# Optimization experiments

Measured on AMD Instinct MI355X. Metric: run time of the kernel, lower is better.

Reference implementation:

```python
import jax, jax.numpy as jnp
import numpy as np


def _three_nn(xyz1, xyz2):
    # xyz1: [B,N1,3], xyz2: [B,N2,3]
    # Squared euclidean distances, as in the original three_nn CUDA/TF op.
    d2 = (jnp.sum(xyz1 * xyz1, axis=-1)[:, :, None]
          + jnp.sum(xyz2 * xyz2, axis=-1)[:, None, :]
          - 2.0 * jnp.einsum('bnd,bmd->bnm', xyz1, xyz2))  # [B,N1,N2]
    neg_vals, idx = jax.lax.top_k(-d2, 3)                 # 3 smallest
    return -neg_vals, idx                                  # dist [B,N1,3], idx [B,N1,3]


def reference(xyz1, xyz2, points1, points2, w1, w2):
    dist, idx = _three_nn(xyz1, xyz2)
    dist = jnp.maximum(dist, 1e-10)
    inv = 1.0 / dist                                       # [B,N1,3]
    weight = inv / jnp.sum(inv, axis=2, keepdims=True)     # [B,N1,3]

    B = points2.shape[0]
    b_idx = jnp.arange(B)[:, None, None]
    gathered = points2[b_idx, idx]                         # [B,N1,3,C2]
    interpolated = jnp.einsum('bnk,bnkc->bnc', weight, gathered)  # [B,N1,C2]

    new_points = jnp.concatenate([interpolated, points1], axis=2)  # [B,N1,C2+C1]

    # 1x1 conv MLP = per-point matmul; bn=False, activation=relu on all layers
    h = jax.nn.relu(jnp.einsum('bnc,cf->bnf', new_points, w1))
    h = jax.nn.relu(jnp.einsum('bnc,cf->bnf', h, w2))
    return h


def setup_inputs() -> dict:
    key = jax.random.key(0)
    k1, k2, k3, k4, k5, k6 = jax.random.split(key, 6)
    B, N1, N2, C1, C2 = 4, 8192, 2048, 128, 256
    xyz1 = jax.random.normal(k1, (B, N1, 3), dtype=jnp.float32)
    xyz2 = jax.random.normal(k2, (B, N2, 3), dtype=jnp.float32)
    points1 = jax.random.normal(k3, (B, N1, C1), dtype=jnp.float32)
    points2 = jax.random.normal(k4, (B, N2, C2), dtype=jnp.float32)
    # glorot-normal-ish init for the 1x1 conv kernels
    w1 = jax.random.normal(k5, (C2 + C1, 256), dtype=jnp.float32) * (2.0 / (C2 + C1 + 256)) ** 0.5
    w2 = jax.random.normal(k6, (256, 256), dtype=jnp.float32) * (2.0 / (256 + 256)) ** 0.5
    return {"xyz1": xyz1, "xyz2": xyz2, "points1": points1, "points2": points2, "w1": w1, "w2": w2}
```

## Files before the change

### kernel.cpp

```cpp
#include <hip/hip_runtime.h>
#include <stdint.h>

typedef unsigned short u16;
typedef unsigned int   u32;

#define NB 4
#define N1 8192
#define N2 2048
#define C1 128
#define C2 256
#define KK1 384
#define FF 256
#define TM 64
#define NTHR 1024
#define NCH 16
#define CHSZ (N2 / NCH)
#define TILES_PER_B (N1 / TM)
#define APAD 400
#define HPAD 272
#define NKT1 (KK1 / 32)
#define NKT2 (FF / 32)
#define ABYTES (TM * APAD * 2)
#define PDOFF  ABYTES
#define PIOFF  (ABYTES + NCH * TM * 3 * 4)

typedef short short8 __attribute__((ext_vector_type(8)));
typedef float floatx4 __attribute__((ext_vector_type(4)));
typedef float f32x2  __attribute__((ext_vector_type(2)));
typedef u32   u32x4  __attribute__((ext_vector_type(4)));

union ABFrag { u32 u[4]; short8 v; u32x4 q; };

__device__ __forceinline__ u16 f2b(float f) {
    u32 x = __float_as_uint(f);
    return (u16)((x + 0x7FFFu + ((x >> 16) & 1u)) >> 16);
}
__device__ __forceinline__ u32 pack2(float a, float b) {
    return (u32)f2b(a) | ((u32)f2b(b) << 16);
}

__global__ __launch_bounds__(256) void prep_kernel(
    const float* __restrict__ w1, const float* __restrict__ w2,
    const float* __restrict__ xyz2,
    u32x4* __restrict__ w1F, u32x4* __restrict__ w2F, float* __restrict__ xq)
{
    int i = blockIdx.x * 256 + threadIdx.x;
    if (i < 16 * NKT1 * 64) {
        int nt = i / (NKT1 * 64), rem = i % (NKT1 * 64);
        int kt = rem / 64, lane = rem % 64;
        int n  = nt * 16 + (lane & 15);
        int k0 = kt * 32 + (lane >> 4) * 8;
        const float* wc = w1 + n;
        ABFrag f;
        f.u[0] = pack2(wc[(k0 + 0) * FF], wc[(k0 + 1) * FF]);
        f.u[1] = pack2(wc[(k0 + 2) * FF], wc[(k0 + 3) * FF]);
        f.u[2] = pack2(wc[(k0 + 4) * FF], wc[(k0 + 5) * FF]);
        f.u[3] = pack2(wc[(k0 + 6) * FF], wc[(k0 + 7) * FF]);
        w1F[i] = f.q;
        return;
    }
    i -= 16 * NKT1 * 64;
    if (i < 16 * NKT2 * 64) {
        int nt = i / (NKT2 * 64), rem = i % (NKT2 * 64);
        int kt = rem / 64, lane = rem % 64;
        int n  = nt * 16 + (lane & 15);
        int k0 = kt * 32 + (lane >> 4) * 8;
        const float* wc = w2 + n;
        ABFrag f;
        f.u[0] = pack2(wc[(k0 + 0) * FF], wc[(k0 + 1) * FF]);
        f.u[1] = pack2(wc[(k0 + 2) * FF], wc[(k0 + 3) * FF]);
        f.u[2] = pack2(wc[(k0 + 4) * FF], wc[(k0 + 5) * FF]);
        f.u[3] = pack2(wc[(k0 + 6) * FF], wc[(k0 + 7) * FF]);
        w2F[i] = f.q;
        return;
    }
    i -= 16 * NKT2 * 64;
    if (i < NB * N2) {
        const float* q = xyz2 + (size_t)i * 3;
        float x = q[0], y = q[1], z = q[2];
        float s2 = __fadd_rn(__fadd_rn(__fmul_rn(x,x), __fmul_rn(y,y)), __fmul_rn(z,z));
        int p = i >> 1, e = i & 1;
        float* rec = xq + (size_t)p * 8;
        rec[0 + e] = -2.0f * x;
        rec[2 + e] = -2.0f * y;
        rec[4 + e] = -2.0f * z;
        rec[6 + e] = s2;
    }
}

__global__ __launch_bounds__(NTHR, 8) void fp_fused_kernel(
    const float* __restrict__ xyz1, const float* __restrict__ p1,
    const float* __restrict__ p2,
    const u32x4* __restrict__ w1F,  const u32x4* __restrict__ w2F,
    const float4* __restrict__ xq,  float* __restrict__ out)
{
    __shared__ int   s_idx[TM][3];
    __shared__ float s_wt[TM][3];
    __shared__ __align__(16) char s_buf[ABYTES + NCH * TM * 3 * 8];

    const int tid = threadIdx.x;
    const int b   = blockIdx.x / TILES_PER_B;
    const int t0  = (blockIdx.x % TILES_PER_B) * TM;

    u16*   A  = (u16*)s_buf;
    float* pd = (float*)(s_buf + PDOFF);
    int*   pi = (int*)(s_buf + PIOFF);

    {
        const int c4 = (tid & 31) * 4, r32 = tid >> 5;
        #pragma unroll
        for (int rv = 0; rv < 2; ++rv) {
            int rr = r32 + rv * 32;
            float4 v = *(const float4*)(p1 + ((size_t)b * N1 + t0 + rr) * C1 + c4);
            u32* w = (u32*)(A + rr * APAD + 256 + c4);
            w[0] = pack2(v.x, v.y);
            w[1] = pack2(v.z, v.w);
        }
    }

    {
        const int r  = tid & 63;
        const int ch = __builtin_amdgcn_readfirstlane(tid >> 6);
        const float4* cb = xq + ((size_t)b * (N2 / 2) + ch * (CHSZ / 2)) * 2;
        const float* q = xyz1 + ((size_t)b * N1 + t0 + r) * 3;
        float qx = q[0], qy = q[1], qz = q[2];
        float s1 = __fadd_rn(__fadd_rn(__fmul_rn(qx,qx), __fmul_rn(qy,qy)), __fmul_rn(qz,qz));
        float bd0 = 3e38f, bd1 = 3e38f, bd2 = 3e38f;
        int   bi0 = 0, bi1 = 0, bi2 = 0;
        const int j0 = ch * CHSZ;
        #pragma unroll 4
        for (int jj = 0; jj < CHSZ / 2; ++jj) {
            float4 f0 = cb[2 * jj];
            float4 f1 = cb[2 * jj + 1];
            f32x2 dpair;
            {
                #pragma clang fp contract(off)
                f32x2 qx2 = {qx, qx}, qy2 = {qy, qy}, qz2 = {qz, qz}, s1v = {s1, s1};
                f32x2 nx = {f0.x, f0.y}, ny = {f0.z, f0.w};
                f32x2 nz = {f1.x, f1.y}, ss = {f1.z, f1.w};
                f32x2 u  = qx2 * nx;
                f32x2 v  = qy2 * ny;
                f32x2 w  = u + v;
                f32x2 z2 = qz2 * nz;
                f32x2 t  = w + z2;
                f32x2 s12 = s1v + ss;
                dpair = s12 + t;
            }
            #pragma unroll
            for (int e = 0; e < 2; ++e) {
                float d = dpair[e];
                int   j = j0 + 2 * jj + e;
                float nb0 = fminf(d, bd0);
                float nb1 = __builtin_amdgcn_fmed3f(d, bd0, bd1);
                float nb2 = __builtin_amdgcn_fmed3f(d, bd1, bd2);
                bool c0 = d < bd0, c1 = d < bd1, c2 = d < bd2;
                int t01 = c0 ? bi0 : j;
                bi0     = c0 ? j   : bi0;
                int t12 = c1 ? bi1 : j;
                bi1     = c1 ? t01 : bi1;
                bi2     = c2 ? t12 : bi2;
                bd0 = nb0; bd1 = nb1; bd2 = nb2;
            }
        }
        const int o = (ch * TM + r) * 3;
        pd[o+0] = bd0; pd[o+1] = bd1; pd[o+2] = bd2;
        pi[o+0] = bi0; pi[o+1] = bi1; pi[o+2] = bi2;
    }
    __syncthreads();

    if (tid < TM) {
        float d0 = 3e38f, d1 = 3e38f, d2 = 3e38f;
        int   i0 = 0, i1 = 0, i2 = 0;
        for (int c = 0; c < NCH; ++c) {
            const int o = (c * TM + tid) * 3;
            #pragma unroll
            for (int k = 0; k < 3; ++k) {
                float d = pd[o + k]; int ix = pi[o + k];
                float n0 = fminf(d, d0);
                float n1 = __builtin_amdgcn_fmed3f(d, d0, d1);
                float n2 = __builtin_amdgcn_fmed3f(d, d1, d2);
                bool c0 = d < d0, c1 = d < d1, c2 = d < d2;
                int t01 = c0 ? i0 : ix;
                i0      = c0 ? ix : i0;
                int t12 = c1 ? i1 : t01;
                i1      = c1 ? t01 : i1;
                i2      = c2 ? t12 : i2;
                d0 = n0; d1 = n1; d2 = n2;
            }
        }
        d0 = fmaxf(d0, 1e-10f); d1 = fmaxf(d1, 1e-10f); d2 = fmaxf(d2, 1e-10f);
        float v0 = 1.0f / d0, v1 = 1.0f / d1, v2 = 1.0f / d2;
        float s  = 1.0f / (v0 + v1 + v2);
        s_wt[tid][0] = v0 * s; s_wt[tid][1] = v1 * s; s_wt[tid][2] = v2 * s;
        s_idx[tid][0] = i0; s_idx[tid][1] = i1; s_idx[tid][2] = i2;
    }
    __syncthreads();

    {
        const float* pb = p2 + (size_t)b * N2 * C2;
        const int col4 = (tid & 63) * 4;
        const int wvr  = tid >> 6;
        #pragma unroll
        for (int m = 0; m < 4; ++m) {
            int rr = wvr + m * 16;
            float w0 = s_wt[rr][0], w1v = s_wt[rr][1], w2v = s_wt[rr][2];
            int   i0 = s_idx[rr][0], i1 = s_idx[rr][1], i2 = s_idx[rr][2];
            float4 a0 = *(const float4*)(pb + (size_t)i0 * C2 + col4);
            float4 a1 = *(const float4*)(pb + (size_t)i1 * C2 + col4);
            float4 a2 = *(const float4*)(pb + (size_t)i2 * C2 + col4);
            float e0 = w0 * a0.x + w1v * a1.x + w2v * a2.x;
            float e1 = w0 * a0.y + w1v * a1.y + w2v * a2.y;
            float e2 = w0 * a0.z + w1v * a1.z + w2v * a2.z;
            float e3 = w0 * a0.w + w1v * a1.w + w2v * a2.w;
            u32* w = (u32*)(A + rr * APAD + col4);
            w[0] = pack2(e0, e1);
            w[1] = pack2(e2, e3);
        }
    }
    __syncthreads();

    const int lane = tid & 63;
    const int wv   = tid >> 6;
    const int lr   = lane & 15;
    const int lg   = lane >> 4;
    const int wvb  = wv * 16;

    int id1[4], id2[4];
    {
        u16 rbf = f2b((float)lr);
        u16 c32 = f2b(1.0f / 32.0f);
        ABFrag pa, pc;
        u32 ra = (u32)rbf | ((u32)rbf << 16);
        u32 rc = (u32)c32 | ((u32)c32 << 16);
        pa.u[0] = pa.u[1] = pa.u[2] = pa.u[3] = ra;
        pc.u[0] = pc.u[1] = pc.u[2] = pc.u[3] = rc;
        floatx4 z = {0.f, 0.f, 0.f, 0.f};
        floatx4 D1 = __builtin_amdgcn_mfma_f32_16x16x32_bf16(pa.v, pc.v, z, 0, 0, 0);
        floatx4 D2 = __builtin_amdgcn_mfma_f32_16x16x32_bf16(pc.v, pa.v, z, 0, 0, 0);
        #pragma unroll
        for (int g = 0; g < 4; ++g) { id1[g] = (int)(D1[g] + 0.5f); id2[g] = (int)(D2[g] + 0.5f); }
    }

    floatx4 acc[4];
    #pragma unroll
    for (int i = 0; i < 4; ++i) acc[i] = floatx4{0.f, 0.f, 0.f, 0.f};

    {
        const u32x4* wf = w1F + (size_t)(wv * NKT1) * 64 + lane;
        const int kb8 = lg * 8;
        for (int kk = 0; kk < NKT1; ++kk) {
            ABFrag bf; bf.q = wf[(size_t)kk * 64];
            ABFrag a[4];
            #pragma unroll
            for (int rt = 0; rt < 4; ++rt)
                a[rt].q = *(const u32x4*)(A + (rt * 16 + lr) * APAD + kk * 32 + kb8);
            #pragma unroll
            for (int rt = 0; rt < 4; ++rt)
                acc[rt] = __builtin_amdgcn_mfma_f32_16x16x32_bf16(a[rt].v, bf.v, acc[rt], 0, 0, 0);
        }
    }
    __syncthreads();

    u16* H = (u16*)s_buf;
    #pragma unroll
    for (int rt = 0; rt < 4; ++rt)
        #pragma unroll
        for (int g = 0; g < 4; ++g) {
            int row = rt * 16 + id1[g];
            int col = wvb + id2[g];
            H[row * HPAD + col] = f2b(fmaxf(acc[rt][g], 0.0f));
        }
    __syncthreads();

    floatx4 acc2[4];
    #pragma unroll
    for (int i = 0; i < 4; ++i) acc2[i] = floatx4{0.f, 0.f, 0.f, 0.f};

    {
        const u32x4* wf = w2F + (size_t)(wv * NKT2) * 64 + lane;
        const int kb8 = lg * 8;
        for (int kk = 0; kk < NKT2; ++kk) {
            ABFrag bf; bf.q = wf[(size_t)kk * 64];
            ABFrag a[4];
            #pragma unroll
            for (int rt = 0; rt < 4; ++rt)
                a[rt].q = *(const u32x4*)(H + (rt * 16 + lr) * HPAD + kk * 32 + kb8);
            #pragma unroll
            for (int rt = 0; rt < 4; ++rt)
                acc2[rt] = __builtin_amdgcn_mfma_f32_16x16x32_bf16(a[rt].v, bf.v, acc2[rt], 0, 0, 0);
        }
    }

    float* ob = out + ((size_t)b * N1 + t0) * FF;
    #pragma unroll
    for (int rt = 0; rt < 4; ++rt)
        #pragma unroll
        for (int g = 0; g < 4; ++g) {
            int row = rt * 16 + id1[g];
            int col = wvb + id2[g];
            ob[(size_t)row * FF + col] = fmaxf(acc2[rt][g], 0.0f);
        }
}

extern "C" void kernel_launch(void* const* d_in, const int* in_sizes, int n_in,
                              void* d_out, int out_size, void* d_ws, size_t ws_size,
                              hipStream_t stream)
{
    (void)in_sizes; (void)n_in; (void)out_size; (void)ws_size;
    const float* xyz1 = (const float*)d_in[0];
    const float* xyz2 = (const float*)d_in[1];
    const float* p1   = (const float*)d_in[2];
    const float* p2   = (const float*)d_in[3];
    const float* w1   = (const float*)d_in[4];
    const float* w2   = (const float*)d_in[5];
    float* out = (float*)d_out;

    u32x4* w1F = (u32x4*)d_ws;
    u32x4* w2F = w1F + 16 * NKT1 * 64;
    float* xqw = (float*)(w2F + 16 * NKT2 * 64);

    int prep_items = 16 * NKT1 * 64 + 16 * NKT2 * 64 + NB * N2;
    prep_kernel<<<(prep_items + 255) / 256, 256, 0, stream>>>(w1, w2, xyz2, w1F, w2F, xqw);
    fp_fused_kernel<<<NB * TILES_PER_B, NTHR, 0, stream>>>(
        xyz1, p1, p2, w1F, w2F, (const float4*)xqw, out);
}
```

Baseline: 62.75 us.

## Split fused kernel into separate kNN and MLP GEMM kernels

Splits the single 1024-thread fused kernel into a 256-thread kNN kernel (4 chunks per tile) and a 512-thread gather+MLP kernel in which each wave computes two 16-column tiles. The kNN weights and indices pass between the kernels through scratch slots in the output buffer, and the second kernel later overwrites those slots. Each stage can now pick its own block size and occupancy, and each wave reuses its A fragments across two column tiles. The cost is an extra launch and a global round trip for the kNN results, and the kNN loop now walks longer serial chunks per thread.

```diff
diff --git a/kernel.cpp b/kernel.cpp
--- a/kernel.cpp
+++ b/kernel.cpp
@@ -12,17 +12,15 @@
 #define KK1 384
 #define FF 256
 #define TM 64
-#define NTHR 1024
-#define NCH 16
-#define CHSZ (N2 / NCH)
 #define TILES_PER_B (N1 / TM)
 #define APAD 400
 #define HPAD 272
 #define NKT1 (KK1 / 32)
 #define NKT2 (FF / 32)
-#define ABYTES (TM * APAD * 2)
-#define PDOFF  ABYTES
-#define PIOFF  (ABYTES + NCH * TM * 3 * 4)
+#define ATHR 256
+#define NCHA 4
+#define CHA  (N2 / NCHA)
+#define BTHR 512
 
 typedef short short8 __attribute__((ext_vector_type(8)));
 typedef float floatx4 __attribute__((ext_vector_type(4)));
@@ -88,48 +86,29 @@
     }
 }
 
-__global__ __launch_bounds__(NTHR, 8) void fp_fused_kernel(
-    const float* __restrict__ xyz1, const float* __restrict__ p1,
-    const float* __restrict__ p2,
-    const u32x4* __restrict__ w1F,  const u32x4* __restrict__ w2F,
-    const float4* __restrict__ xq,  float* __restrict__ out)
+__global__ __launch_bounds__(ATHR, 8) void knn_kernel(
+    const float* __restrict__ xyz1, const float4* __restrict__ xq,
+    float* __restrict__ out)
 {
-    __shared__ int   s_idx[TM][3];
-    __shared__ float s_wt[TM][3];
-    __shared__ __align__(16) char s_buf[ABYTES + NCH * TM * 3 * 8];
+    __shared__ float pd[NCHA][TM][3];
+    __shared__ int   pi[NCHA][TM][3];
 
     const int tid = threadIdx.x;
     const int b   = blockIdx.x / TILES_PER_B;
     const int t0  = (blockIdx.x % TILES_PER_B) * TM;
 
-    u16*   A  = (u16*)s_buf;
-    float* pd = (float*)(s_buf + PDOFF);
-    int*   pi = (int*)(s_buf + PIOFF);
-
-    {
-        const int c4 = (tid & 31) * 4, r32 = tid >> 5;
-        #pragma unroll
-        for (int rv = 0; rv < 2; ++rv) {
-            int rr = r32 + rv * 32;
-            float4 v = *(const float4*)(p1 + ((size_t)b * N1 + t0 + rr) * C1 + c4);
-            u32* w = (u32*)(A + rr * APAD + 256 + c4);
-            w[0] = pack2(v.x, v.y);
-            w[1] = pack2(v.z, v.w);
-        }
-    }
-
     {
         const int r  = tid & 63;
         const int ch = __builtin_amdgcn_readfirstlane(tid >> 6);
-        const float4* cb = xq + ((size_t)b * (N2 / 2) + ch * (CHSZ / 2)) * 2;
+        const float4* cb = xq + ((size_t)b * (N2 / 2) + ch * (CHA / 2)) * 2;
         const float* q = xyz1 + ((size_t)b * N1 + t0 + r) * 3;
         float qx = q[0], qy = q[1], qz = q[2];
         float s1 = __fadd_rn(__fadd_rn(__fmul_rn(qx,qx), __fmul_rn(qy,qy)), __fmul_rn(qz,qz));
         float bd0 = 3e38f, bd1 = 3e38f, bd2 = 3e38f;
         int   bi0 = 0, bi1 = 0, bi2 = 0;
-        const int j0 = ch * CHSZ;
+        const int j0 = ch * CHA;
         #pragma unroll 4
-        for (int jj = 0; jj < CHSZ / 2; ++jj) {
+        for (int jj = 0; jj < CHA / 2; ++jj) {
             float4 f0 = cb[2 * jj];
             float4 f1 = cb[2 * jj + 1];
             f32x2 dpair;
@@ -162,20 +141,18 @@
                 bd0 = nb0; bd1 = nb1; bd2 = nb2;
             }
         }
-        const int o = (ch * TM + r) * 3;
-        pd[o+0] = bd0; pd[o+1] = bd1; pd[o+2] = bd2;
-        pi[o+0] = bi0; pi[o+1] = bi1; pi[o+2] = bi2;
+        pd[ch][tid & 63][0] = bd0; pd[ch][tid & 63][1] = bd1; pd[ch][tid & 63][2] = bd2;
+        pi[ch][tid & 63][0] = bi0; pi[ch][tid & 63][1] = bi1; pi[ch][tid & 63][2] = bi2;
     }
     __syncthreads();
 
     if (tid < TM) {
         float d0 = 3e38f, d1 = 3e38f, d2 = 3e38f;
         int   i0 = 0, i1 = 0, i2 = 0;
-        for (int c = 0; c < NCH; ++c) {
-            const int o = (c * TM + tid) * 3;
+        for (int c = 0; c < NCHA; ++c) {
             #pragma unroll
             for (int k = 0; k < 3; ++k) {
-                float d = pd[o + k]; int ix = pi[o + k];
+                float d = pd[c][tid][k]; int ix = pi[c][tid][k];
                 float n0 = fminf(d, d0);
                 float n1 = __builtin_amdgcn_fmed3f(d, d0, d1);
                 float n2 = __builtin_amdgcn_fmed3f(d, d1, d2);
@@ -191,8 +168,48 @@
         d0 = fmaxf(d0, 1e-10f); d1 = fmaxf(d1, 1e-10f); d2 = fmaxf(d2, 1e-10f);
         float v0 = 1.0f / d0, v1 = 1.0f / d1, v2 = 1.0f / d2;
         float s  = 1.0f / (v0 + v1 + v2);
-        s_wt[tid][0] = v0 * s; s_wt[tid][1] = v1 * s; s_wt[tid][2] = v2 * s;
-        s_idx[tid][0] = i0; s_idx[tid][1] = i1; s_idx[tid][2] = i2;
+        float* rec = out + ((size_t)(b * N1 + t0 + tid) * FF + 248);
+        *(float4*)(rec)     = make_float4(v0 * s, v1 * s, v2 * s, 0.0f);
+        *(float4*)(rec + 4) = make_float4(__int_as_float(i0), __int_as_float(i1),
+                                          __int_as_float(i2), 0.0f);
+    }
+}
+
+__global__ __launch_bounds__(BTHR, 4) void fp_gemm_kernel(
+    const float* __restrict__ p1, const float* __restrict__ p2,
+    const u32x4* __restrict__ w1F, const u32x4* __restrict__ w2F,
+    float* __restrict__ out)
+{
+    __shared__ int   s_idx[TM][3];
+    __shared__ float s_wt[TM][3];
+    __shared__ __align__(16) char s_buf[TM * APAD * 2];
+
+    const int tid = threadIdx.x;
+    const int b   = blockIdx.x / TILES_PER_B;
+    const int t0  = (blockIdx.x % TILES_PER_B) * TM;
+
+    u16* A = (u16*)s_buf;
+
+    if (tid < TM) {
+        const float* rec = out + ((size_t)(b * N1 + t0 + tid) * FF + 248);
+        float4 a0 = *(const float4*)(rec);
+        float4 a1 = *(const float4*)(rec + 4);
+        s_wt[tid][0] = a0.x; s_wt[tid][1] = a0.y; s_wt[tid][2] = a0.z;
+        s_idx[tid][0] = __float_as_int(a1.x);
+        s_idx[tid][1] = __float_as_int(a1.y);
+        s_idx[tid][2] = __float_as_int(a1.z);
+    }
+
+    {
+        const int c4 = (tid & 31) * 4, r16 = tid >> 5;
+        #pragma unroll
+        for (int rv = 0; rv < 4; ++rv) {
+            int rr = r16 + rv * 16;
+            float4 v = *(const float4*)(p1 + ((size_t)b * N1 + t0 + rr) * C1 + c4);
+            u32* w = (u32*)(A + rr * APAD + 256 + c4);
+            w[0] = pack2(v.x, v.y);
+            w[1] = pack2(v.z, v.w);
+        }
     }
     __syncthreads();
 
@@ -201,8 +218,8 @@
         const int col4 = (tid & 63) * 4;
         const int wvr  = tid >> 6;
         #pragma unroll
-        for (int m = 0; m < 4; ++m) {
-            int rr = wvr + m * 16;
+        for (int m = 0; m < 8; ++m) {
+            int rr = wvr + m * 8;
             float w0 = s_wt[rr][0], w1v = s_wt[rr][1], w2v = s_wt[rr][2];
             int   i0 = s_idx[rr][0], i1 = s_idx[rr][1], i2 = s_idx[rr][2];
             float4 a0 = *(const float4*)(pb + (size_t)i0 * C2 + col4);
@@ -223,7 +240,7 @@
     const int wv   = tid >> 6;
     const int lr   = lane & 15;
     const int lg   = lane >> 4;
-    const int wvb  = wv * 16;
+    const int kb8  = lg * 8;
 
     int id1[4], id2[4];
     {
@@ -241,22 +258,23 @@
         for (int g = 0; g < 4; ++g) { id1[g] = (int)(D1[g] + 0.5f); id2[g] = (int)(D2[g] + 0.5f); }
     }
 
-    floatx4 acc[4];
+    floatx4 acc[4][2];
     #pragma unroll
-    for (int i = 0; i < 4; ++i) acc[i] = floatx4{0.f, 0.f, 0.f, 0.f};
-
-    {
-        const u32x4* wf = w1F + (size_t)(wv * NKT1) * 64 + lane;
-        const int kb8 = lg * 8;
-        for (int kk = 0; kk < NKT1; ++kk) {
-            ABFrag bf; bf.q = wf[(size_t)kk * 64];
-            ABFrag a[4];
+    for (int i = 0; i < 4; ++i)
+        #pragma unroll
+        for (int j = 0; j < 2; ++j) acc[i][j] = floatx4{0.f, 0.f, 0.f, 0.f};
+
+    for (int kk = 0; kk < NKT1; ++kk) {
+        ABFrag a[4];
+        #pragma unroll
+        for (int rt = 0; rt < 4; ++rt)
+            a[rt].q = *(const u32x4*)(A + (rt * 16 + lr) * APAD + kk * 32 + kb8);
+        #pragma unroll
+        for (int ct = 0; ct < 2; ++ct) {
+            ABFrag bf; bf.q = w1F[(size_t)((wv * 2 + ct) * NKT1 + kk) * 64 + lane];
             #pragma unroll
             for (int rt = 0; rt < 4; ++rt)
-                a[rt].q = *(const u32x4*)(A + (rt * 16 + lr) * APAD + kk * 32 + kb8);
-            #pragma unroll
-            for (int rt = 0; rt < 4; ++rt)
-                acc[rt] = __builtin_amdgcn_mfma_f32_16x16x32_bf16(a[rt].v, bf.v, acc[rt], 0, 0, 0);
+                acc[rt][ct] = __builtin_amdgcn_mfma_f32_16x16x32_bf16(a[rt].v, bf.v, acc[rt][ct], 0, 0, 0);
         }
     }
     __syncthreads();
@@ -265,29 +283,32 @@
     #pragma unroll
     for (int rt = 0; rt < 4; ++rt)
         #pragma unroll
-        for (int g = 0; g < 4; ++g) {
-            int row = rt * 16 + id1[g];
-            int col = wvb + id2[g];
-            H[row * HPAD + col] = f2b(fmaxf(acc[rt][g], 0.0f));
-        }
-    __syncthreads();
-
-    floatx4 acc2[4];
+        for (int ct = 0; ct < 2; ++ct)
+            #pragma unroll
+            for (int g = 0; g < 4; ++g) {
+                int row = rt * 16 + id1[g];
+                int col = wv * 32 + ct * 16 + id2[g];
+                H[row * HPAD + col] = f2b(fmaxf(acc[rt][ct][g], 0.0f));
+            }
+    __syncthreads();
+
+    floatx4 acc2[4][2];
     #pragma unroll
-    for (int i = 0; i < 4; ++i) acc2[i] = floatx4{0.f, 0.f, 0.f, 0.f};
-
-    {
-        const u32x4* wf = w2F + (size_t)(wv * NKT2) * 64 + lane;
-        const int kb8 = lg * 8;
-        for (int kk = 0; kk < NKT2; ++kk) {
-            ABFrag bf; bf.q = wf[(size_t)kk * 64];
-            ABFrag a[4];
+    for (int i = 0; i < 4; ++i)
+        #pragma unroll
+        for (int j = 0; j < 2; ++j) acc2[i][j] = floatx4{0.f, 0.f, 0.f, 0.f};
+
+    for (int kk = 0; kk < NKT2; ++kk) {
+        ABFrag a[4];
+        #pragma unroll
+        for (int rt = 0; rt < 4; ++rt)
+            a[rt].q = *(const u32x4*)(H + (rt * 16 + lr) * HPAD + kk * 32 + kb8);
+        #pragma unroll
+        for (int ct = 0; ct < 2; ++ct) {
+            ABFrag bf; bf.q = w2F[(size_t)((wv * 2 + ct) * NKT2 + kk) * 64 + lane];
             #pragma unroll
             for (int rt = 0; rt < 4; ++rt)
-                a[rt].q = *(const u32x4*)(H + (rt * 16 + lr) * HPAD + kk * 32 + kb8);
-            #pragma unroll
-            for (int rt = 0; rt < 4; ++rt)
-                acc2[rt] = __builtin_amdgcn_mfma_f32_16x16x32_bf16(a[rt].v, bf.v, acc2[rt], 0, 0, 0);
+                acc2[rt][ct] = __builtin_amdgcn_mfma_f32_16x16x32_bf16(a[rt].v, bf.v, acc2[rt][ct], 0, 0, 0);
         }
     }
 
@@ -295,11 +316,13 @@
     #pragma unroll
     for (int rt = 0; rt < 4; ++rt)
         #pragma unroll
-        for (int g = 0; g < 4; ++g) {
-            int row = rt * 16 + id1[g];
-            int col = wvb + id2[g];
-            ob[(size_t)row * FF + col] = fmaxf(acc2[rt][g], 0.0f);
-        }
+        for (int ct = 0; ct < 2; ++ct)
+            #pragma unroll
+            for (int g = 0; g < 4; ++g) {
+                int row = rt * 16 + id1[g];
+                int col = wv * 32 + ct * 16 + id2[g];
+                ob[(size_t)row * FF + col] = fmaxf(acc2[rt][ct][g], 0.0f);
+            }
 }
 
 extern "C" void kernel_launch(void* const* d_in, const int* in_sizes, int n_in,
@@ -321,6 +344,6 @@
 
     int prep_items = 16 * NKT1 * 64 + 16 * NKT2 * 64 + NB * N2;
     prep_kernel<<<(prep_items + 255) / 256, 256, 0, stream>>>(w1, w2, xyz2, w1F, w2F, xqw);
-    fp_fused_kernel<<<NB * TILES_PER_B, NTHR, 0, stream>>>(
-        xyz1, p1, p2, w1F, w2F, (const float4*)xqw, out);
-}
+    knn_kernel<<<NB * TILES_PER_B, ATHR, 0, stream>>>(xyz1, (const float4*)xqw, out);
+    fp_gemm_kernel<<<NB * TILES_PER_B, BTHR, 0, stream>>>(p1, p2, w1F, w2F, out);
+}
```

Measured after the change: 74.94 us. +19.4%, slower.

## Halve row tile to 32 points with 512 threads and 2x2 MFMA warp tiles

Applied to the files above, without the earlier changes.

Shrinks the per-block tile from 64 to 32 query points and the block from 1024 to 512 threads, doubling the grid. Each wave now computes a 2x2 grid of 16x16 MFMA tiles (two row tiles by two column tiles), reusing each A fragment across two weight fragments, instead of four row tiles against one column tile. The point-to-wave mapping in the nearest-neighbour search changes from 64 lanes per chunk to 32, and that loop's unroll goes from 4 to 8. More blocks should improve CU load balance and latency hiding, but each block now reloads the full weight matrices for half as many rows, doubling global weight traffic per output point.

```diff
diff --git a/kernel.cpp b/kernel.cpp
--- a/kernel.cpp
+++ b/kernel.cpp
@@ -11,8 +11,8 @@
 #define C2 256
 #define KK1 384
 #define FF 256
-#define TM 64
-#define NTHR 1024
+#define TM 32
+#define NTHR 512
 #define NCH 16
 #define CHSZ (N2 / NCH)
 #define TILES_PER_B (N1 / TM)
@@ -22,7 +22,6 @@
 #define NKT2 (FF / 32)
 #define ABYTES (TM * APAD * 2)
 #define PDOFF  ABYTES
-#define PIOFF  (ABYTES + NCH * TM * 3 * 4)
 
 typedef short short8 __attribute__((ext_vector_type(8)));
 typedef float floatx4 __attribute__((ext_vector_type(4)));
@@ -104,13 +103,13 @@
 
     u16*   A  = (u16*)s_buf;
     float* pd = (float*)(s_buf + PDOFF);
-    int*   pi = (int*)(s_buf + PIOFF);
+    int*   pi = (int*)(s_buf + PDOFF + NCH * TM * 3 * 4);
 
     {
-        const int c4 = (tid & 31) * 4, r32 = tid >> 5;
+        const int c4 = (tid & 31) * 4, r16 = tid >> 5;
         #pragma unroll
         for (int rv = 0; rv < 2; ++rv) {
-            int rr = r32 + rv * 32;
+            int rr = r16 + rv * 16;
             float4 v = *(const float4*)(p1 + ((size_t)b * N1 + t0 + rr) * C1 + c4);
             u32* w = (u32*)(A + rr * APAD + 256 + c4);
             w[0] = pack2(v.x, v.y);
@@ -119,8 +118,8 @@
     }
 
     {
-        const int r  = tid & 63;
-        const int ch = __builtin_amdgcn_readfirstlane(tid >> 6);
+        const int r  = tid & 31;
+        const int ch = tid >> 5;
         const float4* cb = xq + ((size_t)b * (N2 / 2) + ch * (CHSZ / 2)) * 2;
         const float* q = xyz1 + ((size_t)b * N1 + t0 + r) * 3;
         float qx = q[0], qy = q[1], qz = q[2];
@@ -128,7 +127,7 @@
         float bd0 = 3e38f, bd1 = 3e38f, bd2 = 3e38f;
         int   bi0 = 0, bi1 = 0, bi2 = 0;
         const int j0 = ch * CHSZ;
-        #pragma unroll 4
+        #pragma unroll 8
         for (int jj = 0; jj < CHSZ / 2; ++jj) {
             float4 f0 = cb[2 * jj];
             float4 f1 = cb[2 * jj + 1];
@@ -202,7 +201,7 @@
         const int wvr  = tid >> 6;
         #pragma unroll
         for (int m = 0; m < 4; ++m) {
-            int rr = wvr + m * 16;
+            int rr = wvr + m * 8;
             float w0 = s_wt[rr][0], w1v = s_wt[rr][1], w2v = s_wt[rr][2];
             int   i0 = s_idx[rr][0], i1 = s_idx[rr][1], i2 = s_idx[rr][2];
             float4 a0 = *(const float4*)(pb + (size_t)i0 * C2 + col4);
@@ -223,7 +222,7 @@
     const int wv   = tid >> 6;
     const int lr   = lane & 15;
     const int lg   = lane >> 4;
-    const int wvb  = wv * 16;
+    const int kb8  = lg * 8;
 
     int id1[4], id2[4];
     {
@@ -241,65 +240,71 @@
         for (int g = 0; g < 4; ++g) { id1[g] = (int)(D1[g] + 0.5f); id2[g] = (int)(D2[g] + 0.5f); }
     }
 
-    floatx4 acc[4];
+    floatx4 acc[2][2];
     #pragma unroll
-    for (int i = 0; i < 4; ++i) acc[i] = floatx4{0.f, 0.f, 0.f, 0.f};
-
-    {
-        const u32x4* wf = w1F + (size_t)(wv * NKT1) * 64 + lane;
-        const int kb8 = lg * 8;
-        for (int kk = 0; kk < NKT1; ++kk) {
-            ABFrag bf; bf.q = wf[(size_t)kk * 64];
-            ABFrag a[4];
-            #pragma unroll
-            for (int rt = 0; rt < 4; ++rt)
-                a[rt].q = *(const u32x4*)(A + (rt * 16 + lr) * APAD + kk * 32 + kb8);
-            #pragma unroll
-            for (int rt = 0; rt < 4; ++rt)
-                acc[rt] = __builtin_amdgcn_mfma_f32_16x16x32_bf16(a[rt].v, bf.v, acc[rt], 0, 0, 0);
+    for (int i = 0; i < 2; ++i)
+        #pragma unroll
+        for (int j = 0; j < 2; ++j) acc[i][j] = floatx4{0.f, 0.f, 0.f, 0.f};
+
+    for (int kk = 0; kk < NKT1; ++kk) {
+        ABFrag a[2];
+        #pragma unroll
+        for (int rt = 0; rt < 2; ++rt)
+            a[rt].q = *(const u32x4*)(A + (rt * 16 + lr) * APAD + kk * 32 + kb8);
+        #pragma unroll
+        for (int ct = 0; ct < 2; ++ct) {
+            ABFrag bf; bf.q = w1F[(size_t)((wv * 2 + ct) * NKT1 + kk) * 64 + lane];
+            #pragma unroll
+            for (int rt = 0; rt < 2; ++rt)
+                acc[rt][ct] = __builtin_amdgcn_mfma_f32_16x16x32_bf16(a[rt].v, bf.v, acc[rt][ct], 0, 0, 0);
         }
     }
     __syncthreads();
 
     u16* H = (u16*)s_buf;
     #pragma unroll
-    for (int rt = 0; rt < 4; ++rt)
-        #pragma unroll
-        for (int g = 0; g < 4; ++g) {
-            int row = rt * 16 + id1[g];
-            int col = wvb + id2[g];
-            H[row * HPAD + col] = f2b(fmaxf(acc[rt][g], 0.0f));
-        }
-    __syncthreads();
-
-    floatx4 acc2[4];
+    for (int rt = 0; rt < 2; ++rt)
+        #pragma unroll
+        for (int ct = 0; ct < 2; ++ct)
+            #pragma unroll
+            for (int g = 0; g < 4; ++g) {
+                int row = rt * 16 + id1[g];
+                int col = wv * 32 + ct * 16 + id2[g];
+                H[row * HPAD + col] = f2b(fmaxf(acc[rt][ct][g], 0.0f));
+            }
+    __syncthreads();
+
+    floatx4 acc2[2][2];
     #pragma unroll
-    for (int i = 0; i < 4; ++i) acc2[i] = floatx4{0.f, 0.f, 0.f, 0.f};
-
-    {
-        const u32x4* wf = w2F + (size_t)(wv * NKT2) * 64 + lane;
-        const int kb8 = lg * 8;
-        for (int kk = 0; kk < NKT2; ++kk) {
-            ABFrag bf; bf.q = wf[(size_t)kk * 64];
-            ABFrag a[4];
-            #pragma unroll
-            for (int rt = 0; rt < 4; ++rt)
-                a[rt].q = *(const u32x4*)(H + (rt * 16 + lr) * HPAD + kk * 32 + kb8);
-            #pragma unroll
-            for (int rt = 0; rt < 4; ++rt)
-                acc2[rt] = __builtin_amdgcn_mfma_f32_16x16x32_bf16(a[rt].v, bf.v, acc2[rt], 0, 0, 0);
+    for (int i = 0; i < 2; ++i)
+        #pragma unroll
+        for (int j = 0; j < 2; ++j) acc2[i][j] = floatx4{0.f, 0.f, 0.f, 0.f};
+
+    for (int kk = 0; kk < NKT2; ++kk) {
+        ABFrag a[2];
+        #pragma unroll
+        for (int rt = 0; rt < 2; ++rt)
+            a[rt].q = *(const u32x4*)(H + (rt * 16 + lr) * HPAD + kk * 32 + kb8);
+        #pragma unroll
+        for (int ct = 0; ct < 2; ++ct) {
+            ABFrag bf; bf.q = w2F[(size_t)((wv * 2 + ct) * NKT2 + kk) * 64 + lane];
+            #pragma unroll
+            for (int rt = 0; rt < 2; ++rt)
+                acc2[rt][ct] = __builtin_amdgcn_mfma_f32_16x16x32_bf16(a[rt].v, bf.v, acc2[rt][ct], 0, 0, 0);
         }
     }
 
     float* ob = out + ((size_t)b * N1 + t0) * FF;
     #pragma unroll
-    for (int rt = 0; rt < 4; ++rt)
-        #pragma unroll
-        for (int g = 0; g < 4; ++g) {
-            int row = rt * 16 + id1[g];
-            int col = wvb + id2[g];
-            ob[(size_t)row * FF + col] = fmaxf(acc2[rt][g], 0.0f);
-        }
+    for (int rt = 0; rt < 2; ++rt)
+        #pragma unroll
+        for (int ct = 0; ct < 2; ++ct)
+            #pragma unroll
+            for (int g = 0; g < 4; ++g) {
+                int row = rt * 16 + id1[g];
+                int col = wv * 32 + ct * 16 + id2[g];
+                ob[(size_t)row * FF + col] = fmaxf(acc2[rt][ct][g], 0.0f);
+            }
 }
 
 extern "C" void kernel_launch(void* const* d_in, const int* in_sizes, int n_in,
```

Result: slower. 65.50 us (+4.4%).

## Split nearest-neighbour scan into two halves and prune the second with a bound

Applied to the files above, without the earlier changes.

The three-nearest-neighbour search now runs in two passes. The first pass scans half of the candidate points and merges the per-wave results. Its third-best distance then seeds the second pass, and a wave skips the top-3 insertion work whenever no lane's candidate beats its current bound. This is meant to cut the compare/select cost of the neighbour search, at the price of an extra barrier, a second merge and divergent branches. The bf16 packing also switches to a single hardware convert instruction.

```diff
diff --git a/kernel.cpp b/kernel.cpp
--- a/kernel.cpp
+++ b/kernel.cpp
@@ -14,15 +14,13 @@
 #define TM 64
 #define NTHR 1024
 #define NCH 16
-#define CHSZ (N2 / NCH)
+#define HALF 1024
+#define SUB 64
 #define TILES_PER_B (N1 / TM)
 #define APAD 400
 #define HPAD 272
 #define NKT1 (KK1 / 32)
 #define NKT2 (FF / 32)
-#define ABYTES (TM * APAD * 2)
-#define PDOFF  ABYTES
-#define PIOFF  (ABYTES + NCH * TM * 3 * 4)
 
 typedef short short8 __attribute__((ext_vector_type(8)));
 typedef float floatx4 __attribute__((ext_vector_type(4)));
@@ -36,7 +34,9 @@
     return (u16)((x + 0x7FFFu + ((x >> 16) & 1u)) >> 16);
 }
 __device__ __forceinline__ u32 pack2(float a, float b) {
-    return (u32)f2b(a) | ((u32)f2b(b) << 16);
+    u32 r;
+    asm("v_cvt_pk_bf16_f32 %0, %1, %2" : "=v"(r) : "v"(a), "v"(b));
+    return r;
 }
 
 __global__ __launch_bounds__(256) void prep_kernel(
@@ -96,15 +96,15 @@
 {
     __shared__ int   s_idx[TM][3];
     __shared__ float s_wt[TM][3];
-    __shared__ __align__(16) char s_buf[ABYTES + NCH * TM * 3 * 8];
+    __shared__ float s_m[TM][8];
+    __shared__ float s_pd[NCH * TM * 3];
+    __shared__ int   s_pi[NCH * TM * 3];
+    __shared__ __align__(16) char s_buf[TM * APAD * 2];
 
     const int tid = threadIdx.x;
     const int b   = blockIdx.x / TILES_PER_B;
     const int t0  = (blockIdx.x % TILES_PER_B) * TM;
-
-    u16*   A  = (u16*)s_buf;
-    float* pd = (float*)(s_buf + PDOFF);
-    int*   pi = (int*)(s_buf + PIOFF);
+    u16* A = (u16*)s_buf;
 
     {
         const int c4 = (tid & 31) * 4, r32 = tid >> 5;
@@ -118,18 +118,20 @@
         }
     }
 
-    {
-        const int r  = tid & 63;
-        const int ch = __builtin_amdgcn_readfirstlane(tid >> 6);
-        const float4* cb = xq + ((size_t)b * (N2 / 2) + ch * (CHSZ / 2)) * 2;
-        const float* q = xyz1 + ((size_t)b * N1 + t0 + r) * 3;
-        float qx = q[0], qy = q[1], qz = q[2];
-        float s1 = __fadd_rn(__fadd_rn(__fmul_rn(qx,qx), __fmul_rn(qy,qy)), __fmul_rn(qz,qz));
+    const int r  = tid & 63;
+    const int ch = __builtin_amdgcn_readfirstlane(tid >> 6);
+
+    const float* q = xyz1 + ((size_t)b * N1 + t0 + r) * 3;
+    const float qx = q[0], qy = q[1], qz = q[2];
+    const float s1 = __fadd_rn(__fadd_rn(__fmul_rn(qx,qx), __fmul_rn(qy,qy)), __fmul_rn(qz,qz));
+
+    {
+        const float4* cb = xq + ((size_t)b * (N2 / 2) + ch * (SUB / 2)) * 2;
         float bd0 = 3e38f, bd1 = 3e38f, bd2 = 3e38f;
-        int   bi0 = 0, bi1 = 0, bi2 = 0;
-        const int j0 = ch * CHSZ;
-        #pragma unroll 4
-        for (int jj = 0; jj < CHSZ / 2; ++jj) {
+        int   bi0 = -1, bi1 = -1, bi2 = -1;
+        const int j0 = ch * SUB;
+        #pragma unroll 8
+        for (int jj = 0; jj < SUB / 2; ++jj) {
             float4 f0 = cb[2 * jj];
             float4 f1 = cb[2 * jj + 1];
             f32x2 dpair;
@@ -163,19 +165,96 @@
             }
         }
         const int o = (ch * TM + r) * 3;
-        pd[o+0] = bd0; pd[o+1] = bd1; pd[o+2] = bd2;
-        pi[o+0] = bi0; pi[o+1] = bi1; pi[o+2] = bi2;
+        s_pd[o+0] = bd0; s_pd[o+1] = bd1; s_pd[o+2] = bd2;
+        s_pi[o+0] = bi0; s_pi[o+1] = bi1; s_pi[o+2] = bi2;
     }
     __syncthreads();
 
     if (tid < TM) {
         float d0 = 3e38f, d1 = 3e38f, d2 = 3e38f;
-        int   i0 = 0, i1 = 0, i2 = 0;
+        int   i0 = -1, i1 = -1, i2 = -1;
         for (int c = 0; c < NCH; ++c) {
             const int o = (c * TM + tid) * 3;
             #pragma unroll
             for (int k = 0; k < 3; ++k) {
-                float d = pd[o + k]; int ix = pi[o + k];
+                float d = s_pd[o + k]; int ix = s_pi[o + k];
+                float n0 = fminf(d, d0);
+                float n1 = __builtin_amdgcn_fmed3f(d, d0, d1);
+                float n2 = __builtin_amdgcn_fmed3f(d, d1, d2);
+                bool c0 = d < d0, c1 = d < d1, c2 = d < d2;
+                int t01 = c0 ? i0 : ix;
+                i0      = c0 ? ix : i0;
+                int t12 = c1 ? i1 : t01;
+                i1      = c1 ? t01 : i1;
+                i2      = c2 ? t12 : i2;
+                d0 = n0; d1 = n1; d2 = n2;
+            }
+        }
+        s_m[tid][0] = d0; s_m[tid][1] = d1; s_m[tid][2] = d2;
+        s_m[tid][4] = __int_as_float(i0);
+        s_m[tid][5] = __int_as_float(i1);
+        s_m[tid][6] = __int_as_float(i2);
+    }
+    __syncthreads();
+
+    {
+        const float bound = s_m[r][2];
+        const float4* cb = xq + ((size_t)b * (N2 / 2) + (HALF / 2) + ch * (SUB / 2)) * 2;
+        float bd0 = bound, bd1 = bound, bd2 = bound;
+        int   bi0 = -1, bi1 = -1, bi2 = -1;
+        const int j0 = HALF + ch * SUB;
+        #pragma unroll 4
+        for (int jj = 0; jj < SUB / 2; ++jj) {
+            float4 f0 = cb[2 * jj];
+            float4 f1 = cb[2 * jj + 1];
+            f32x2 dpair;
+            {
+                #pragma clang fp contract(off)
+                f32x2 qx2 = {qx, qx}, qy2 = {qy, qy}, qz2 = {qz, qz}, s1v = {s1, s1};
+                f32x2 nx = {f0.x, f0.y}, ny = {f0.z, f0.w};
+                f32x2 nz = {f1.x, f1.y}, ss = {f1.z, f1.w};
+                f32x2 u  = qx2 * nx;
+                f32x2 v  = qy2 * ny;
+                f32x2 w  = u + v;
+                f32x2 z2 = qz2 * nz;
+                f32x2 t  = w + z2;
+                f32x2 s12 = s1v + ss;
+                dpair = s12 + t;
+            }
+            if (__any((dpair.x < bd2) || (dpair.y < bd2))) {
+                #pragma unroll
+                for (int e = 0; e < 2; ++e) {
+                    float d = dpair[e];
+                    int   j = j0 + 2 * jj + e;
+                    float nb0 = fminf(d, bd0);
+                    float nb1 = __builtin_amdgcn_fmed3f(d, bd0, bd1);
+                    float nb2 = __builtin_amdgcn_fmed3f(d, bd1, bd2);
+                    bool c0 = d < bd0, c1 = d < bd1, c2 = d < bd2;
+                    int t01 = c0 ? bi0 : j;
+                    bi0     = c0 ? j   : bi0;
+                    int t12 = c1 ? bi1 : j;
+                    bi1     = c1 ? t01 : bi1;
+                    bi2     = c2 ? t12 : bi2;
+                    bd0 = nb0; bd1 = nb1; bd2 = nb2;
+                }
+            }
+        }
+        const int o = (ch * TM + r) * 3;
+        s_pd[o+0] = bd0; s_pd[o+1] = bd1; s_pd[o+2] = bd2;
+        s_pi[o+0] = bi0; s_pi[o+1] = bi1; s_pi[o+2] = bi2;
+    }
+    __syncthreads();
+
+    if (tid < TM) {
+        float d0 = s_m[tid][0], d1 = s_m[tid][1], d2 = s_m[tid][2];
+        int   i0 = __float_as_int(s_m[tid][4]);
+        int   i1 = __float_as_int(s_m[tid][5]);
+        int   i2 = __float_as_int(s_m[tid][6]);
+        for (int c = 0; c < NCH; ++c) {
+            const int o = (c * TM + tid) * 3;
+            #pragma unroll
+            for (int k = 0; k < 3; ++k) {
+                float d = s_pd[o + k]; int ix = s_pi[o + k];
                 float n0 = fminf(d, d0);
                 float n1 = __builtin_amdgcn_fmed3f(d, d0, d1);
                 float n2 = __builtin_amdgcn_fmed3f(d, d1, d2);
@@ -223,6 +302,7 @@
     const int wv   = tid >> 6;
     const int lr   = lane & 15;
     const int lg   = lane >> 4;
+    const int kb8  = lg * 8;
     const int wvb  = wv * 16;
 
     int id1[4], id2[4];
@@ -244,10 +324,8 @@
     floatx4 acc[4];
     #pragma unroll
     for (int i = 0; i < 4; ++i) acc[i] = floatx4{0.f, 0.f, 0.f, 0.f};
-
     {
         const u32x4* wf = w1F + (size_t)(wv * NKT1) * 64 + lane;
-        const int kb8 = lg * 8;
         for (int kk = 0; kk < NKT1; ++kk) {
             ABFrag bf; bf.q = wf[(size_t)kk * 64];
             ABFrag a[4];
@@ -275,10 +353,8 @@
     floatx4 acc2[4];
     #pragma unroll
     for (int i = 0; i < 4; ++i) acc2[i] = floatx4{0.f, 0.f, 0.f, 0.f};
-
     {
         const u32x4* wf = w2F + (size_t)(wv * NKT2) * 64 + lane;
-        const int kb8 = lg * 8;
         for (int kk = 0; kk < NKT2; ++kk) {
             ABFrag bf; bf.q = wf[(size_t)kk * 64];
             ABFrag a[4];
```

New measurement: 60.96 us. 2.9% less time.
